# Performance work log

Measured on AMD Instinct MI355X. Metric: run time of the kernel, lower is better.

The kernel has to match this reference:

```python
import jax, jax.numpy as jnp
import numpy as np

B, H, W, K, PAD = 1024, 28, 28, 3, 1


def conv3x3(x, w, b):
    out = jax.lax.conv_general_dilated(x, w, (1, 1), ((PAD, PAD), (PAD, PAD)),
                                       dimension_numbers=('NCHW', 'OIHW', 'NCHW'))
    return out + b[None, :, None, None]


def deform_conv2d(x, offset, w, b):
    # torchvision deform_conv2d semantics, stride=1, pad=1, dilation=1, groups=1
    Bn, Cin, Hh, Ww = x.shape
    Cout = w.shape[0]
    KK = K * K
    off = offset.reshape(Bn, KK, 2, Hh, Ww)
    dy, dx = off[:, :, 0], off[:, :, 1]                      # [B,KK,H,W]
    ky, kx = jnp.meshgrid(jnp.arange(K, dtype=x.dtype), jnp.arange(K, dtype=x.dtype), indexing='ij')
    py = dy + (jnp.arange(Hh, dtype=x.dtype) - PAD)[None, None, :, None] + ky.reshape(KK)[None, :, None, None]
    px = dx + (jnp.arange(Ww, dtype=x.dtype) - PAD)[None, None, None, :] + kx.reshape(KK)[None, :, None, None]
    y0 = jnp.floor(py); x0 = jnp.floor(px)
    wy1 = py - y0; wy0 = 1.0 - wy1
    wx1 = px - x0; wx0 = 1.0 - wx1
    xf = x.reshape(Bn, Cin, Hh * Ww)

    def gather(yi, xi):
        valid = (yi >= 0) & (yi < Hh) & (xi >= 0) & (xi < Ww)
        yc = jnp.clip(yi, 0, Hh - 1).astype(jnp.int32)
        xc = jnp.clip(xi, 0, Ww - 1).astype(jnp.int32)
        idx = (yc * Ww + xc).reshape(Bn, -1)                 # [B, KK*H*W]
        g = jnp.take_along_axis(xf, jnp.broadcast_to(idx[:, None, :], (Bn, Cin, idx.shape[1])), axis=2)
        return g.reshape(Bn, Cin, KK, Hh, Ww) * valid.astype(x.dtype)[:, None]

    sampled = (gather(y0, x0) * (wy0 * wx0)[:, None]
               + gather(y0, x0 + 1) * (wy0 * wx1)[:, None]
               + gather(y0 + 1, x0) * (wy1 * wx0)[:, None]
               + gather(y0 + 1, x0 + 1) * (wy1 * wx1)[:, None])  # [B,Cin,KK,H,W]
    out = jnp.einsum('bkhw,ok->bohw', sampled.reshape(Bn, Cin * KK, Hh, Ww),
                     w.reshape(Cout, Cin * KK))
    return out + b[None, :, None, None]


def adaptive_avg_pool_14(x):
    Bn, C, Hh, Ww = x.shape
    f = Hh // 14
    return x.reshape(Bn, C, 14, f, 14, f).mean(axis=(3, 5))


def setup_inputs() -> dict:
    key = jax.random.key(0)
    ks = jax.random.split(key, 14)
    d = {}
    d['x'] = jax.random.normal(ks[0], (B, 1, H, W), dtype=jnp.float32)
    # offset conv 1: Conv2d(1, 18, 3, pad=1)
    d['ow1'] = jax.random.normal(ks[1], (18, 1, 3, 3), dtype=jnp.float32) * 0.1
    d['ob1'] = jnp.zeros((18,), jnp.float32)
    d['w1'] = jax.random.normal(ks[2], (32, 1, 3, 3), dtype=jnp.float32) * 0.01
    d['b1'] = jnp.zeros((32,), jnp.float32)
    # offset conv 2: Conv2d(32, 18, 3, pad=1)
    d['ow2'] = jax.random.normal(ks[3], (18, 32, 3, 3), dtype=jnp.float32) * 0.05
    d['ob2'] = jnp.zeros((18,), jnp.float32)
    d['w2'] = jax.random.normal(ks[4], (64, 32, 3, 3), dtype=jnp.float32) * 0.01
    d['b2'] = jnp.zeros((64,), jnp.float32)
    d['fw1'] = jax.random.normal(ks[5], (128, 64 * 14 * 14), dtype=jnp.float32) * 0.01
    d['fb1'] = jnp.zeros((128,), jnp.float32)
    d['fw2'] = jax.random.normal(ks[6], (10, 128), dtype=jnp.float32) * 0.05
    d['fb2'] = jnp.zeros((10,), jnp.float32)
    return d


def reference(x, ow1, ob1, w1, b1, ow2, ob2, w2, b2, fw1, fb1, fw2, fb2):
    # block1 + relu + pool 28->14
    h = deform_conv2d(x, conv3x3(x, ow1, ob1), w1, b1)
    h = adaptive_avg_pool_14(jax.nn.relu(h))
    # block2 + relu + pool 14->14 (identity)
    h = deform_conv2d(h, conv3x3(h, ow2, ob2), w2, b2)
    h = adaptive_avg_pool_14(jax.nn.relu(h))
    h = h.reshape(h.shape[0], -1)
    # classifier (ExcitationDropout is identity in eval mode)
    h = jax.nn.relu(h @ fw1.T + fb1)
    return h @ fw2.T + fb2
```

## Files before the change

kernel.cpp:

```cpp
#include <hip/hip_runtime.h>

#define NB 1024
#define TOTAL1 (NB*196)
#define SPS 200

#define WS_H1   0
#define WS_H2   6422528
#define WS_PART 19267584
#define WS_W1T  23461888
#define WS_OW1T 23462176
#define WS_W2T  23462338
#define WS_OW2T 23480770

__global__ __launch_bounds__(256) void prep(const float* __restrict__ w1,
                                            const float* __restrict__ ow1,
                                            const float* __restrict__ w2,
                                            const float* __restrict__ ow2,
                                            float* __restrict__ ws) {
  int i = blockIdx.x * 256 + threadIdx.x;
  if (i < 288)   { int co = i / 9,  kk = i % 9;   ws[WS_W1T  + kk * 32 + co] = w1[i]; }
  if (i < 162)   { int c  = i / 9,  j  = i % 9;   ws[WS_OW1T + j  * 18 + c ] = ow1[i]; }
  if (i < 18432) { int co = i / 288, k = i % 288; ws[WS_W2T  + k  * 64 + co] = w2[i]; }
  if (i < 5184)  { int c  = i / 288, k = i % 288; ws[WS_OW2T + k  * 18 + c ] = ow2[i]; }
}

__global__ __launch_bounds__(256, 2) void stage1(const float* __restrict__ x,
                                                 const float* __restrict__ ob1,
                                                 const float* __restrict__ b1,
                                                 const float* __restrict__ ws,
                                                 float* __restrict__ h1) {
  __shared__ float ximg[3 * 784];
  const float* __restrict__ w1t  = ws + WS_W1T;
  const float* __restrict__ ow1t = ws + WS_OW1T;
  int tid = threadIdx.x;
  int g0 = blockIdx.x * 256;
  int bfirst = g0 / 196;
  for (int idx = tid; idx < 3 * 784; idx += 256) {
    int img = idx / 784;
    int b = bfirst + img;
    ximg[idx] = (b < NB) ? x[b * 784 + (idx - img * 784)] : 0.f;
  }
  __syncthreads();
  int g = g0 + tid;
  if (g >= TOTAL1) return;
  int b = g / 196, p = g - b * 196;
  const float* im = ximg + (b - bfirst) * 784;
  int oy = p / 14, ox = p - (p / 14) * 14;

  float pooled[32];
#pragma unroll
  for (int co = 0; co < 32; ++co) pooled[co] = 0.f;

  for (int sub = 0; sub < 4; ++sub) {
    int y  = 2 * oy + (sub >> 1);
    int ix = 2 * ox + (sub & 1);
    float patch[9];
#pragma unroll
    for (int j = 0; j < 9; ++j) {
      int yy = y + j / 3 - 1, xc = ix + j % 3 - 1;
      bool ok = (yy >= 0) & (yy < 28) & (xc >= 0) & (xc < 28);
      patch[j] = ok ? im[yy * 28 + xc] : 0.f;
    }
    float off[18];
#pragma unroll
    for (int c = 0; c < 18; ++c) off[c] = ob1[c];
#pragma unroll
    for (int j = 0; j < 9; ++j) {
      float v = patch[j];
#pragma unroll
      for (int c = 0; c < 18; ++c) off[c] = fmaf(v, ow1t[j * 18 + c], off[c]);
    }
    float a[32];
#pragma unroll
    for (int co = 0; co < 32; ++co) a[co] = b1[co];
#pragma unroll
    for (int kk = 0; kk < 9; ++kk) {
      float py = (float)(y - 1 + kk / 3) + off[2 * kk];
      float px = (float)(ix - 1 + kk % 3) + off[2 * kk + 1];
      float y0f = floorf(py), x0f = floorf(px);
      float wy1 = py - y0f, wx1 = px - x0f;
      float wy0 = 1.f - wy1, wx0 = 1.f - wx1;
      int y0 = (int)y0f, x0 = (int)x0f;
      int y1 = y0 + 1, x1 = x0 + 1;
      bool vy0 = (y0 >= 0) & (y0 < 28), vy1 = (y1 >= 0) & (y1 < 28);
      bool vx0 = (x0 >= 0) & (x0 < 28), vx1 = (x1 >= 0) & (x1 < 28);
      float W00 = (vy0 & vx0) ? wy0 * wx0 : 0.f;
      float W01 = (vy0 & vx1) ? wy0 * wx1 : 0.f;
      float W10 = (vy1 & vx0) ? wy1 * wx0 : 0.f;
      float W11 = (vy1 & vx1) ? wy1 * wx1 : 0.f;
      int yc0 = min(max(y0, 0), 27), yc1 = min(max(y1, 0), 27);
      int xc0 = min(max(x0, 0), 27), xc1 = min(max(x1, 0), 27);
      float s = im[yc0 * 28 + xc0] * W00 + im[yc0 * 28 + xc1] * W01 +
                im[yc1 * 28 + xc0] * W10 + im[yc1 * 28 + xc1] * W11;
#pragma unroll
      for (int co = 0; co < 32; ++co) a[co] = fmaf(s, w1t[kk * 32 + co], a[co]);
    }
#pragma unroll
    for (int co = 0; co < 32; ++co) pooled[co] += fmaxf(a[co], 0.f);
  }
#pragma unroll
  for (int co = 0; co < 32; ++co) h1[b * 6272 + co * 196 + p] = pooled[co] * 0.25f;
}

__global__ __launch_bounds__(256, 4) void stage2(const float* __restrict__ h1,
                                                 const float* __restrict__ ob2,
                                                 const float* __restrict__ b2,
                                                 const float* __restrict__ ws,
                                                 float* __restrict__ h2) {
  __shared__ float imgT[196 * 32];
  __shared__ float Sbuf[16 * SPS + 8];
  __shared__ float offT[2 * 208];
  const float* __restrict__ w2t  = ws + WS_W2T;
  const float* __restrict__ ow2t = ws + WS_OW2T;
  int tid = threadIdx.x;
  int b = blockIdx.x;

  for (int e = tid; e < 6272; e += 256) {
    int ci = e / 196, p = e - ci * 196;
    imgT[p * 32 + ((ci + 4 * p) & 31)] = h1[b * 6272 + e];
  }
  if (tid < 64) Sbuf[(tid >> 2) * SPS + 196 + (tid & 3)] = 0.f;
  if (tid < 8)  Sbuf[16 * SPS + tid] = 0.f;

  int pp = tid;
  int spy = pp / 14, spx = pp - (pp / 14) * 14;

  int oc  = tid % 18;
  int opg = tid / 18;
  int op0 = opg * 16;
  bool oact = (tid < 234);
  float oacc[16];
#pragma unroll
  for (int i = 0; i < 16; ++i) oacc[i] = 0.f;

  for (int j = 0; j < 9; ++j) {
    for (int h = 0; h < 2; ++h) {
      __syncthreads();
      if (pp < 196) {
        int yy = spy + j / 3 - 1, xx = spx + j % 3 - 1;
        bool ok = (yy >= 0) & (yy < 14) & (xx >= 0) & (xx < 14);
        int idx = ok ? (yy * 14 + xx) : 0;
        const float* src = imgT + idx * 32;
        int rot = (4 * idx) & 31;
#pragma unroll
        for (int cg = 0; cg < 4; ++cg) {
          int cgg = h * 4 + cg;
          float4 v;
          if (ok) v = *(const float4*)(src + ((cgg * 4 + rot) & 31));
          else    v = make_float4(0.f, 0.f, 0.f, 0.f);
          Sbuf[(cg * 4 + 0) * SPS + pp] = v.x;
          Sbuf[(cg * 4 + 1) * SPS + pp] = v.y;
          Sbuf[(cg * 4 + 2) * SPS + pp] = v.z;
          Sbuf[(cg * 4 + 3) * SPS + pp] = v.w;
        }
      }
      __syncthreads();
      if (oact) {
        float wv[16];
#pragma unroll
        for (int l = 0; l < 16; ++l) wv[l] = ow2t[((h * 16 + l) * 9 + j) * 18 + oc];
        for (int l = 0; l < 16; ++l) {
          const float* srow = Sbuf + l * SPS + op0;
          float w = wv[l];
#pragma unroll
          for (int t = 0; t < 4; ++t) {
            float4 s = *(const float4*)(srow + 4 * t);
            oacc[4 * t + 0] = fmaf(w, s.x, oacc[4 * t + 0]);
            oacc[4 * t + 1] = fmaf(w, s.y, oacc[4 * t + 1]);
            oacc[4 * t + 2] = fmaf(w, s.z, oacc[4 * t + 2]);
            oacc[4 * t + 3] = fmaf(w, s.w, oacc[4 * t + 3]);
          }
        }
      }
    }
  }

  int cog = tid & 15, pg = tid >> 4;
  int co0 = cog * 4;
  int p0 = pg * 16;
  bool gact = (pg < 13);
  float acc[4][16];
  {
    float4 bb = *(const float4*)(b2 + co0);
    float bj[4] = {bb.x, bb.y, bb.z, bb.w};
#pragma unroll
    for (int jj = 0; jj < 4; ++jj)
#pragma unroll
      for (int i = 0; i < 16; ++i) acc[jj][i] = bj[jj];
  }
  float myob = oact ? ob2[oc] : 0.f;

  for (int kk = 0; kk < 9; ++kk) {
    __syncthreads();
    if (oact && (oc >> 1) == kk) {
      float* dst = offT + (oc & 1) * 208 + op0;
#pragma unroll
      for (int i = 0; i < 16; ++i) dst[i] = oacc[i] + myob;
    }
    __syncthreads();
    for (int h = 0; h < 2; ++h) {
      if (h == 1) __syncthreads();
      if (pp < 196) {
        float dyv = offT[pp];
        float dxv = offT[208 + pp];
        float pyv = (float)(spy - 1 + kk / 3) + dyv;
        float pxv = (float)(spx - 1 + kk % 3) + dxv;
        float y0f = floorf(pyv), x0f = floorf(pxv);
        float wy1 = pyv - y0f, wx1 = pxv - x0f;
        float wy0 = 1.f - wy1, wx0 = 1.f - wx1;
        int y0 = (int)y0f, x0 = (int)x0f;
        int y1 = y0 + 1, x1 = x0 + 1;
        bool vy0 = (y0 >= 0) & (y0 < 14), vy1 = (y1 >= 0) & (y1 < 14);
        bool vx0 = (x0 >= 0) & (x0 < 14), vx1 = (x1 >= 0) & (x1 < 14);
        float W00 = (vy0 & vx0) ? wy0 * wx0 : 0.f;
        float W01 = (vy0 & vx1) ? wy0 * wx1 : 0.f;
        float W10 = (vy1 & vx0) ? wy1 * wx0 : 0.f;
        float W11 = (vy1 & vx1) ? wy1 * wx1 : 0.f;
        int yc0 = min(max(y0, 0), 13), yc1 = min(max(y1, 0), 13);
        int xc0 = min(max(x0, 0), 13), xc1 = min(max(x1, 0), 13);
        int i00 = yc0 * 14 + xc0, i01 = yc0 * 14 + xc1;
        int i10 = yc1 * 14 + xc0, i11 = yc1 * 14 + xc1;
        const float* s00 = imgT + i00 * 32; int r00 = (4 * i00) & 31;
        const float* s01 = imgT + i01 * 32; int r01 = (4 * i01) & 31;
        const float* s10 = imgT + i10 * 32; int r10 = (4 * i10) & 31;
        const float* s11 = imgT + i11 * 32; int r11 = (4 * i11) & 31;
#pragma unroll
        for (int cg = 0; cg < 4; ++cg) {
          int cgg = h * 4 + cg;
          float4 a0 = *(const float4*)(s00 + ((cgg * 4 + r00) & 31));
          float4 a1 = *(const float4*)(s01 + ((cgg * 4 + r01) & 31));
          float4 a2 = *(const float4*)(s10 + ((cgg * 4 + r10) & 31));
          float4 a3 = *(const float4*)(s11 + ((cgg * 4 + r11) & 31));
          Sbuf[(cg * 4 + 0) * SPS + pp] = fmaf(W00, a0.x, fmaf(W01, a1.x, fmaf(W10, a2.x, W11 * a3.x)));
          Sbuf[(cg * 4 + 1) * SPS + pp] = fmaf(W00, a0.y, fmaf(W01, a1.y, fmaf(W10, a2.y, W11 * a3.y)));
          Sbuf[(cg * 4 + 2) * SPS + pp] = fmaf(W00, a0.z, fmaf(W01, a1.z, fmaf(W10, a2.z, W11 * a3.z)));
          Sbuf[(cg * 4 + 3) * SPS + pp] = fmaf(W00, a0.w, fmaf(W01, a1.w, fmaf(W10, a2.w, W11 * a3.w)));
        }
      }
      __syncthreads();
      if (gact) {
        int hbase = h * 16;
        for (int cb = 0; cb < 16; cb += 4) {
          float4 w[4];
#pragma unroll
          for (int u = 0; u < 4; ++u)
            w[u] = *(const float4*)(w2t + ((hbase + cb + u) * 9 + kk) * 64 + co0);
#pragma unroll
          for (int u = 0; u < 4; ++u) {
            const float* srow = Sbuf + (cb + u) * SPS + p0;
            float4 s0 = *(const float4*)(srow);
            float4 s1 = *(const float4*)(srow + 4);
            float4 s2 = *(const float4*)(srow + 8);
            float4 s3 = *(const float4*)(srow + 12);
            float sv[16] = {s0.x, s0.y, s0.z, s0.w, s1.x, s1.y, s1.z, s1.w,
                            s2.x, s2.y, s2.z, s2.w, s3.x, s3.y, s3.z, s3.w};
            float wj[4] = {w[u].x, w[u].y, w[u].z, w[u].w};
#pragma unroll
            for (int jj = 0; jj < 4; ++jj)
#pragma unroll
              for (int i = 0; i < 16; ++i)
                acc[jj][i] = fmaf(wj[jj], sv[i], acc[jj][i]);
          }
        }
      }
    }
  }

  if (gact) {
    float* __restrict__ orow = h2 + b * 12544 + co0 * 196 + p0;
#pragma unroll
    for (int jj = 0; jj < 4; ++jj) {
#pragma unroll
      for (int t = 0; t < 4; ++t) {
        if (p0 + 4 * t < 196) {
          float4 v;
          v.x = fmaxf(acc[jj][4 * t + 0], 0.f);
          v.y = fmaxf(acc[jj][4 * t + 1], 0.f);
          v.z = fmaxf(acc[jj][4 * t + 2], 0.f);
          v.w = fmaxf(acc[jj][4 * t + 3], 0.f);
          *(float4*)(orow + jj * 196 + 4 * t) = v;
        }
      }
    }
  }
}

__global__ __launch_bounds__(256, 2) void fc1(const float* __restrict__ h2,
                                              const float* __restrict__ fw1,
                                              float* __restrict__ part) {
  __shared__ float a_s[56 * 72];
  __shared__ float b_s[56 * 132];
  int tid = threadIdx.x;
  int rb = (blockIdx.x & 15) * 64;
  int ks = blockIdx.x >> 4;
  int kbase = ks * 392;
  int c0 = (tid & 31) * 4;
  int r0 = (tid >> 5) * 8;

  float acc[8][4];
#pragma unroll
  for (int i = 0; i < 8; ++i)
#pragma unroll
    for (int j = 0; j < 4; ++j) acc[i][j] = 0.f;

  for (int ch = 0; ch < 7; ++ch) {
    int kb = kbase + ch * 56;
    __syncthreads();
#pragma unroll
    for (int t = 0; t < 14; ++t) {
      int idx = t * 256 + tid;
      int r = idx / 56, k = idx - r * 56;
      a_s[k * 72 + r] = h2[(rb + r) * 12544 + kb + k];
    }
#pragma unroll
    for (int t = 0; t < 28; ++t) {
      int idx = t * 256 + tid;
      int c = idx / 56, k = idx - c * 56;
      b_s[k * 132 + c] = fw1[c * 12544 + kb + k];
    }
    __syncthreads();
    for (int k = 0; k < 56; ++k) {
      float4 bv = *(const float4*)&b_s[k * 132 + c0];
      float4 av0 = *(const float4*)&a_s[k * 72 + r0];
      float4 av1 = *(const float4*)&a_s[k * 72 + r0 + 4];
      float av[8] = {av0.x, av0.y, av0.z, av0.w, av1.x, av1.y, av1.z, av1.w};
      float bj[4] = {bv.x, bv.y, bv.z, bv.w};
#pragma unroll
      for (int i = 0; i < 8; ++i)
#pragma unroll
        for (int j = 0; j < 4; ++j) acc[i][j] = fmaf(av[i], bj[j], acc[i][j]);
    }
  }
#pragma unroll
  for (int i = 0; i < 8; ++i) {
    int r = rb + r0 + i;
#pragma unroll
    for (int j = 0; j < 4; ++j)
      part[(ks * 1024 + r) * 128 + c0 + j] = acc[i][j];
  }
}

__global__ __launch_bounds__(128) void fcfinal(const float* __restrict__ part,
                                               const float* __restrict__ fb1,
                                               const float* __restrict__ fw2,
                                               const float* __restrict__ fb2,
                                               float* __restrict__ out) {
  __shared__ float tbuf[128];
  int b = blockIdx.x, c = threadIdx.x;
  float s = fb1[c];
  for (int ks = 0; ks < 32; ++ks) s += part[(ks * 1024 + b) * 128 + c];
  tbuf[c] = fmaxf(s, 0.f);
  __syncthreads();
  if (c < 10) {
    float v = fb2[c];
#pragma unroll
    for (int k = 0; k < 128; ++k) v = fmaf(tbuf[k], fw2[c * 128 + k], v);
    out[b * 10 + c] = v;
  }
}

extern "C" void kernel_launch(void* const* d_in, const int* in_sizes, int n_in,
                              void* d_out, int out_size, void* d_ws, size_t ws_size,
                              hipStream_t stream) {
  const float* x   = (const float*)d_in[0];
  const float* ow1 = (const float*)d_in[1];
  const float* ob1 = (const float*)d_in[2];
  const float* w1  = (const float*)d_in[3];
  const float* b1  = (const float*)d_in[4];
  const float* ow2 = (const float*)d_in[5];
  const float* ob2 = (const float*)d_in[6];
  const float* w2  = (const float*)d_in[7];
  const float* b2  = (const float*)d_in[8];
  const float* fw1 = (const float*)d_in[9];
  const float* fb1 = (const float*)d_in[10];
  const float* fw2 = (const float*)d_in[11];
  const float* fb2 = (const float*)d_in[12];
  float* ws  = (float*)d_ws;
  float* out = (float*)d_out;

  prep<<<72, 256, 0, stream>>>(w1, ow1, w2, ow2, ws);
  stage1<<<784, 256, 0, stream>>>(x, ob1, b1, ws, ws + WS_H1);
  stage2<<<NB, 256, 0, stream>>>(ws + WS_H1, ob2, b2, ws, ws + WS_H2);
  fc1<<<512, 256, 0, stream>>>(ws + WS_H2, fw1, ws + WS_PART);
  fcfinal<<<1024, 128, 0, stream>>>(ws + WS_PART, fb1, fw2, fb2, out);
}
```

Baseline: 389.0 us.

## Split offset conv into own kernel and double-buffer sampling in deform stage

Moves the offset convolution out of stage2 into a separate kernel that writes offsets to the workspace, aliasing the fc partials region. Stage2 then reads offsets from global memory and runs a double-buffered pipeline: bilinear sampling of the next 8-channel group into one shared buffer while the GEMM consumes the other, with coefficients for the next tap computed early. This cuts barriers per tap and overlaps sampling with FMA work, at the cost of an extra launch, reloading h1 into LDS twice, and a global round trip for offsets.

After: 416.6 us. 1.07x slower.

```diff
diff --git a/kernel.cpp b/kernel.cpp
--- a/kernel.cpp
+++ b/kernel.cpp
@@ -7,6 +7,7 @@
 #define WS_H1   0
 #define WS_H2   6422528
 #define WS_PART 19267584
+#define WS_OFF2 WS_PART
 #define WS_W1T  23461888
 #define WS_OW1T 23462176
 #define WS_W2T  23462338
@@ -102,15 +103,12 @@
   for (int co = 0; co < 32; ++co) h1[b * 6272 + co * 196 + p] = pooled[co] * 0.25f;
 }
 
-__global__ __launch_bounds__(256, 4) void stage2(const float* __restrict__ h1,
-                                                 const float* __restrict__ ob2,
-                                                 const float* __restrict__ b2,
-                                                 const float* __restrict__ ws,
-                                                 float* __restrict__ h2) {
+__global__ __launch_bounds__(256, 4) void offconv(const float* __restrict__ h1,
+                                                  const float* __restrict__ ob2,
+                                                  const float* __restrict__ ws,
+                                                  float* __restrict__ off2) {
   __shared__ float imgT[196 * 32];
   __shared__ float Sbuf[16 * SPS + 8];
-  __shared__ float offT[2 * 208];
-  const float* __restrict__ w2t  = ws + WS_W2T;
   const float* __restrict__ ow2t = ws + WS_OW2T;
   int tid = threadIdx.x;
   int b = blockIdx.x;
@@ -124,7 +122,6 @@
 
   int pp = tid;
   int spy = pp / 14, spx = pp - (pp / 14) * 14;
-
   int oc  = tid % 18;
   int opg = tid / 18;
   int op0 = opg * 16;
@@ -175,9 +172,38 @@
     }
   }
 
+  if (oact) {
+    float bias = ob2[oc];
+    float* dst = off2 + b * 3528 + oc * 196;
+#pragma unroll
+    for (int i = 0; i < 16; ++i)
+      if (op0 + i < 196) dst[op0 + i] = oacc[i] + bias;
+  }
+}
+
+__global__ __launch_bounds__(256, 4) void stage2(const float* __restrict__ h1,
+                                                 const float* __restrict__ off2,
+                                                 const float* __restrict__ b2,
+                                                 const float* __restrict__ ws,
+                                                 float* __restrict__ h2) {
+  __shared__ float imgT[196 * 32];
+  __shared__ float Sbuf2[2 * 1608];
+  const float* __restrict__ w2t = ws + WS_W2T;
+  int tid = threadIdx.x;
+  int b = blockIdx.x;
+
+  for (int e = tid; e < 6272; e += 256) {
+    int ci = e / 196, p = e - ci * 196;
+    imgT[p * 32 + ((ci + 4 * p) & 31)] = h1[b * 6272 + e];
+  }
+
+  int pp = tid;
+  int spy = pp / 14, spx = pp - (pp / 14) * 14;
+  bool samp = (pp < 196);
+  const float* off_b = off2 + b * 3528;
+
   int cog = tid & 15, pg = tid >> 4;
-  int co0 = cog * 4;
-  int p0 = pg * 16;
+  int co0 = cog * 4, p0 = pg * 16;
   bool gact = (pg < 13);
   float acc[4][16];
   {
@@ -188,81 +214,91 @@
 #pragma unroll
       for (int i = 0; i < 16; ++i) acc[jj][i] = bj[jj];
   }
-  float myob = oact ? ob2[oc] : 0.f;
+
+  float W00 = 0.f, W01 = 0.f, W10 = 0.f, W11 = 0.f;
+  int s00o = 0, s01o = 0, s10o = 0, s11o = 0;
+  int r00 = 0, r01 = 0, r10 = 0, r11 = 0;
+  float dyn = 0.f, dxn = 0.f;
+
+  auto coeff = [&](int kkv) {
+    float pyv = (float)(spy - 1 + kkv / 3) + dyn;
+    float pxv = (float)(spx - 1 + kkv % 3) + dxn;
+    float y0f = floorf(pyv), x0f = floorf(pxv);
+    float wy1 = pyv - y0f, wx1 = pxv - x0f;
+    float wy0 = 1.f - wy1, wx0 = 1.f - wx1;
+    int y0 = (int)y0f, x0 = (int)x0f;
+    int y1 = y0 + 1, x1 = x0 + 1;
+    bool vy0 = (y0 >= 0) & (y0 < 14), vy1 = (y1 >= 0) & (y1 < 14);
+    bool vx0 = (x0 >= 0) & (x0 < 14), vx1 = (x1 >= 0) & (x1 < 14);
+    W00 = (vy0 & vx0) ? wy0 * wx0 : 0.f;
+    W01 = (vy0 & vx1) ? wy0 * wx1 : 0.f;
+    W10 = (vy1 & vx0) ? wy1 * wx0 : 0.f;
+    W11 = (vy1 & vx1) ? wy1 * wx1 : 0.f;
+    int yc0 = min(max(y0, 0), 13), yc1 = min(max(y1, 0), 13);
+    int xc0 = min(max(x0, 0), 13), xc1 = min(max(x1, 0), 13);
+    int i00 = yc0 * 14 + xc0, i01 = yc0 * 14 + xc1;
+    int i10 = yc1 * 14 + xc0, i11 = yc1 * 14 + xc1;
+    s00o = i00 * 32; r00 = (4 * i00) & 31;
+    s01o = i01 * 32; r01 = (4 * i01) & 31;
+    s10o = i10 * 32; r10 = (4 * i10) & 31;
+    s11o = i11 * 32; r11 = (4 * i11) & 31;
+  };
+
+  auto sample = [&](int qn, int bufn) {
+    float* dst = Sbuf2 + bufn * 1608 + pp;
+#pragma unroll
+    for (int cg = 0; cg < 2; ++cg) {
+      int gq = qn * 2 + cg;
+      float4 a0 = *(const float4*)(imgT + s00o + ((gq * 4 + r00) & 31));
+      float4 a1 = *(const float4*)(imgT + s01o + ((gq * 4 + r01) & 31));
+      float4 a2 = *(const float4*)(imgT + s10o + ((gq * 4 + r10) & 31));
+      float4 a3 = *(const float4*)(imgT + s11o + ((gq * 4 + r11) & 31));
+      dst[(cg * 4 + 0) * 200] = fmaf(W00, a0.x, fmaf(W01, a1.x, fmaf(W10, a2.x, W11 * a3.x)));
+      dst[(cg * 4 + 1) * 200] = fmaf(W00, a0.y, fmaf(W01, a1.y, fmaf(W10, a2.y, W11 * a3.y)));
+      dst[(cg * 4 + 2) * 200] = fmaf(W00, a0.z, fmaf(W01, a1.z, fmaf(W10, a2.z, W11 * a3.z)));
+      dst[(cg * 4 + 3) * 200] = fmaf(W00, a0.w, fmaf(W01, a1.w, fmaf(W10, a2.w, W11 * a3.w)));
+    }
+  };
+
+  if (samp) { dyn = off_b[pp]; dxn = off_b[196 + pp]; }
+  __syncthreads();
+  if (samp) { coeff(0); sample(0, 0); }
+  __syncthreads();
 
   for (int kk = 0; kk < 9; ++kk) {
-    __syncthreads();
-    if (oact && (oc >> 1) == kk) {
-      float* dst = offT + (oc & 1) * 208 + op0;
-#pragma unroll
-      for (int i = 0; i < 16; ++i) dst[i] = oacc[i] + myob;
-    }
-    __syncthreads();
-    for (int h = 0; h < 2; ++h) {
-      if (h == 1) __syncthreads();
-      if (pp < 196) {
-        float dyv = offT[pp];
-        float dxv = offT[208 + pp];
-        float pyv = (float)(spy - 1 + kk / 3) + dyv;
-        float pxv = (float)(spx - 1 + kk % 3) + dxv;
-        float y0f = floorf(pyv), x0f = floorf(pxv);
-        float wy1 = pyv - y0f, wx1 = pxv - x0f;
-        float wy0 = 1.f - wy1, wx0 = 1.f - wx1;
-        int y0 = (int)y0f, x0 = (int)x0f;
-        int y1 = y0 + 1, x1 = x0 + 1;
-        bool vy0 = (y0 >= 0) & (y0 < 14), vy1 = (y1 >= 0) & (y1 < 14);
-        bool vx0 = (x0 >= 0) & (x0 < 14), vx1 = (x1 >= 0) & (x1 < 14);
-        float W00 = (vy0 & vx0) ? wy0 * wx0 : 0.f;
-        float W01 = (vy0 & vx1) ? wy0 * wx1 : 0.f;
-        float W10 = (vy1 & vx0) ? wy1 * wx0 : 0.f;
-        float W11 = (vy1 & vx1) ? wy1 * wx1 : 0.f;
-        int yc0 = min(max(y0, 0), 13), yc1 = min(max(y1, 0), 13);
-        int xc0 = min(max(x0, 0), 13), xc1 = min(max(x1, 0), 13);
-        int i00 = yc0 * 14 + xc0, i01 = yc0 * 14 + xc1;
-        int i10 = yc1 * 14 + xc0, i11 = yc1 * 14 + xc1;
-        const float* s00 = imgT + i00 * 32; int r00 = (4 * i00) & 31;
-        const float* s01 = imgT + i01 * 32; int r01 = (4 * i01) & 31;
-        const float* s10 = imgT + i10 * 32; int r10 = (4 * i10) & 31;
-        const float* s11 = imgT + i11 * 32; int r11 = (4 * i11) & 31;
-#pragma unroll
-        for (int cg = 0; cg < 4; ++cg) {
-          int cgg = h * 4 + cg;
-          float4 a0 = *(const float4*)(s00 + ((cgg * 4 + r00) & 31));
-          float4 a1 = *(const float4*)(s01 + ((cgg * 4 + r01) & 31));
-          float4 a2 = *(const float4*)(s10 + ((cgg * 4 + r10) & 31));
-          float4 a3 = *(const float4*)(s11 + ((cgg * 4 + r11) & 31));
-          Sbuf[(cg * 4 + 0) * SPS + pp] = fmaf(W00, a0.x, fmaf(W01, a1.x, fmaf(W10, a2.x, W11 * a3.x)));
-          Sbuf[(cg * 4 + 1) * SPS + pp] = fmaf(W00, a0.y, fmaf(W01, a1.y, fmaf(W10, a2.y, W11 * a3.y)));
-          Sbuf[(cg * 4 + 2) * SPS + pp] = fmaf(W00, a0.z, fmaf(W01, a1.z, fmaf(W10, a2.z, W11 * a3.z)));
-          Sbuf[(cg * 4 + 3) * SPS + pp] = fmaf(W00, a0.w, fmaf(W01, a1.w, fmaf(W10, a2.w, W11 * a3.w)));
+#pragma unroll
+    for (int q = 0; q < 4; ++q) {
+      if (samp && !((kk == 8) & (q == 3))) {
+        if (q == 1 && kk < 8) {
+          dyn = off_b[(2 * kk + 2) * 196 + pp];
+          dxn = off_b[(2 * kk + 3) * 196 + pp];
+        }
+        if (q == 3) coeff(kk + 1);
+        sample((q + 1) & 3, (q + 1) & 1);
+      }
+      if (gact) {
+        const float* sb = Sbuf2 + (q & 1) * 1608 + p0;
+        const float* wb = w2t + kk * 64 + co0;
+#pragma unroll 2
+        for (int l = 0; l < 8; ++l) {
+          int ci = q * 8 + l;
+          float4 w = *(const float4*)(wb + ci * 576);
+          const float* srow = sb + l * 200;
+          float4 s0 = *(const float4*)(srow);
+          float4 s1 = *(const float4*)(srow + 4);
+          float4 s2 = *(const float4*)(srow + 8);
+          float4 s3 = *(const float4*)(srow + 12);
+          float sv[16] = {s0.x, s0.y, s0.z, s0.w, s1.x, s1.y, s1.z, s1.w,
+                          s2.x, s2.y, s2.z, s2.w, s3.x, s3.y, s3.z, s3.w};
+          float wj[4] = {w.x, w.y, w.z, w.w};
+#pragma unroll
+          for (int jj = 0; jj < 4; ++jj)
+#pragma unroll
+            for (int i = 0; i < 16; ++i)
+              acc[jj][i] = fmaf(wj[jj], sv[i], acc[jj][i]);
         }
       }
       __syncthreads();
-      if (gact) {
-        int hbase = h * 16;
-        for (int cb = 0; cb < 16; cb += 4) {
-          float4 w[4];
-#pragma unroll
-          for (int u = 0; u < 4; ++u)
-            w[u] = *(const float4*)(w2t + ((hbase + cb + u) * 9 + kk) * 64 + co0);
-#pragma unroll
-          for (int u = 0; u < 4; ++u) {
-            const float* srow = Sbuf + (cb + u) * SPS + p0;
-            float4 s0 = *(const float4*)(srow);
-            float4 s1 = *(const float4*)(srow + 4);
-            float4 s2 = *(const float4*)(srow + 8);
-            float4 s3 = *(const float4*)(srow + 12);
-            float sv[16] = {s0.x, s0.y, s0.z, s0.w, s1.x, s1.y, s1.z, s1.w,
-                            s2.x, s2.y, s2.z, s2.w, s3.x, s3.y, s3.z, s3.w};
-            float wj[4] = {w[u].x, w[u].y, w[u].z, w[u].w};
-#pragma unroll
-            for (int jj = 0; jj < 4; ++jj)
-#pragma unroll
-              for (int i = 0; i < 16; ++i)
-                acc[jj][i] = fmaf(wj[jj], sv[i], acc[jj][i]);
-          }
-        }
-      }
     }
   }
 
@@ -380,7 +416,8 @@
 
   prep<<<72, 256, 0, stream>>>(w1, ow1, w2, ow2, ws);
   stage1<<<784, 256, 0, stream>>>(x, ob1, b1, ws, ws + WS_H1);
-  stage2<<<NB, 256, 0, stream>>>(ws + WS_H1, ob2, b2, ws, ws + WS_H2);
+  offconv<<<NB, 256, 0, stream>>>(ws + WS_H1, ob2, ws, ws + WS_OFF2);
+  stage2<<<NB, 256, 0, stream>>>(ws + WS_H1, ws + WS_OFF2, b2, ws, ws + WS_H2);
   fc1<<<512, 256, 0, stream>>>(ws + WS_H2, fw1, ws + WS_PART);
   fcfinal<<<1024, 128, 0, stream>>>(ws + WS_PART, fb1, fw2, fb2, out);
 }
```
